# Optimization experiments

Hardware: AMD Instinct MI355X
Metric: run time of the kernel (lower is better)

## Reference

```python
import jax, jax.numpy as jnp
import numpy as np

D = 768          # n_embd
I = 3072         # moe_intermediate_size (4 * n_embd)
E = 8            # n_routed_experts
K = 2            # num_experts_per_tok
LIMIT = 10.0     # swiglu_limit
VOCAB = 32768


def setup_inputs() -> dict:
    key = jax.random.key(0)
    ks = jax.random.split(key, 10)
    s = 0.02
    return {
        "x": jax.random.normal(ks[0], (1, 2048, D), dtype=jnp.float32),
        "input_ids": jax.random.randint(ks[1], (1, 2048), 0, VOCAB, dtype=jnp.int64),
        "gate_w": jax.random.normal(ks[2], (D, E), dtype=jnp.float32) * s,
        "gate_bias": jnp.zeros((E,), dtype=jnp.float32),
        "w1": jax.random.normal(ks[3], (E, D, I), dtype=jnp.float32) * s,
        "w2": jax.random.normal(ks[4], (E, I, D), dtype=jnp.float32) * s,
        "w3": jax.random.normal(ks[5], (E, D, I), dtype=jnp.float32) * s,
        "w1s": jax.random.normal(ks[6], (D, I), dtype=jnp.float32) * s,
        "w2s": jax.random.normal(ks[7], (I, D), dtype=jnp.float32) * s,
        "w3s": jax.random.normal(ks[8], (D, I), dtype=jnp.float32) * s,
    }


def _expert(xf, W1, W2, W3):
    # SwiGLU with asymmetric clamping, as in DeepSeekExpert (swiglu_limit > 0)
    gate = jnp.minimum(xf @ W1, LIMIT)               # clamp max only
    up = jnp.clip(xf @ W3, -LIMIT, LIMIT)            # clamp both sides
    return (jax.nn.silu(gate) * up) @ W2


def reference(x, input_ids, gate_w, gate_bias, w1, w2, w3, w1s, w2s, w3s):
    B, T, _ = x.shape
    flat = x.reshape(-1, D)                           # [N, D], N = B*T
    N = flat.shape[0]

    # gating: sqrtsoftplus scoring
    scores = jnp.sqrt(jax.nn.softplus(flat @ gate_w))  # [N, E]
    routed_scores = scores + gate_bias                 # gate_bias used only for topk selection
    _, indices = jax.lax.top_k(routed_scores, K)       # [N, K]

    weights = jnp.take_along_axis(scores, indices, axis=1)  # [N, K]
    # norm_topk_prob=True; routed_scaling_factor=1.0
    weights = weights / jnp.clip(weights.sum(axis=-1, keepdims=True), 1e-6)

    # dense combine matrix [N, E] (jit-friendly dispatch/combine)
    combine = jnp.zeros((N, E), dtype=weights.dtype)
    combine = combine.at[jnp.arange(N)[:, None], indices].add(weights)

    # shared expert on all tokens
    y = _expert(flat, w1s, w2s, w3s)                   # [N, D]

    # routed experts: batched grouped GEMM over all tokens, then weighted combine
    gate_h = jnp.minimum(jnp.einsum('td,edi->eti', flat, w1), LIMIT)   # [E, N, I]
    up_h = jnp.clip(jnp.einsum('td,edi->eti', flat, w3), -LIMIT, LIMIT)
    h = jax.nn.silu(gate_h) * up_h                     # [E, N, I]
    out_e = jnp.einsum('eti,eid->etd', h, w2)          # [E, N, D]
    routed = jnp.einsum('etd,te->td', out_e, combine)  # [N, D]

    return (y + routed).reshape(B, T, D)
```

## Files before the change

kernel.cpp:

```cpp
#include <hip/hip_runtime.h>


#define D_ 768
#define I_ 3072
#define E_ 8
#define NTOK 2048
#define NPMAX 5120
#define MAXTILES 40
#define NSHT 16

typedef __bf16 bf16x8 __attribute__((ext_vector_type(8)));
typedef float floatx4 __attribute__((ext_vector_type(4)));

__device__ __forceinline__ unsigned short f2b(float f) {
    unsigned int u = __float_as_uint(f);
    u += 0x7fffu + ((u >> 16) & 1u);
    return (unsigned short)(u >> 16);
}


__global__ void tcast_kernel(const float* __restrict__ src,
                             unsigned short* __restrict__ dst, int R, int C) {
    __shared__ float t[32][33];
    const float* s = src + (size_t)blockIdx.z * R * C;
    unsigned short* d = dst + (size_t)blockIdx.z * R * C;
    int c0 = blockIdx.x * 32, r0 = blockIdx.y * 32;
    int tx = threadIdx.x & 31, ty = threadIdx.x >> 5;
#pragma unroll
    for (int j = 0; j < 4; j++) {
        int r = ty + j * 8;
        t[r][tx] = s[(size_t)(r0 + r) * C + c0 + tx];
    }
    __syncthreads();
#pragma unroll
    for (int j = 0; j < 4; j++) {
        int c = ty + j * 8;
        d[(size_t)(c0 + c) * R + r0 + tx] = f2b(t[tx][c]);
    }
}

__global__ void cast_x_kernel(const float* __restrict__ x,
                              unsigned short* __restrict__ xb) {
    int gid = blockIdx.x * 256 + threadIdx.x;
    float4 v = *(const float4*)(x + (size_t)gid * 4);
    ushort4 o;
    o.x = f2b(v.x); o.y = f2b(v.y); o.z = f2b(v.z); o.w = f2b(v.w);
    *(ushort4*)(xb + (size_t)gid * 4) = o;
}


__global__ void gate_topk_kernel(const float* __restrict__ x,
                                 const float* __restrict__ gw,
                                 const float* __restrict__ gb,
                                 int* __restrict__ idx, float* __restrict__ wts) {
    int t = blockIdx.x * 4 + (threadIdx.x >> 6);
    int lane = threadIdx.x & 63;
    float z[E_];
#pragma unroll
    for (int e = 0; e < E_; e++) z[e] = 0.f;
    const float* xr = x + (size_t)t * D_;
    for (int j = lane; j < D_; j += 64) {
        float xv = xr[j];
        const float* g = gw + (size_t)j * E_;
#pragma unroll
        for (int e = 0; e < E_; e++) z[e] += xv * g[e];
    }
#pragma unroll
    for (int off = 32; off > 0; off >>= 1)
#pragma unroll
        for (int e = 0; e < E_; e++) z[e] += __shfl_down(z[e], off, 64);
    if (lane == 0) {
        float s[E_], r[E_];
#pragma unroll
        for (int e = 0; e < E_; e++) {
            float zz = z[e];
            float sp = zz > 0.f ? zz + log1pf(expf(-zz)) : log1pf(expf(zz));
            s[e] = sqrtf(sp);
            r[e] = s[e] + gb[e];
        }
        int i0 = 0;
        for (int e = 1; e < E_; e++) if (r[e] > r[i0]) i0 = e;
        int i1 = (i0 == 0) ? 1 : 0;
        for (int e = 0; e < E_; e++) if (e != i0 && r[e] > r[i1]) i1 = e;
        float w0 = s[i0], w1 = s[i1];
        float inv = 1.f / fmaxf(w0 + w1, 1e-6f);
        idx[2 * t] = i0; idx[2 * t + 1] = i1;
        wts[2 * t] = w0 * inv; wts[2 * t + 1] = w1 * inv;
    }
}


__global__ void route_build_kernel(const int* __restrict__ idx,
                                   const float* __restrict__ wts,
                                   int* __restrict__ pair_token,
                                   float* __restrict__ pair_w,
                                   int* __restrict__ pos_of,
                                   int* __restrict__ tiles) {
    __shared__ int cnt[E_], seg[E_], cur[E_];
    int tid = threadIdx.x;
    if (tid < E_) { cnt[tid] = 0; cur[tid] = 0; }
    __syncthreads();
    for (int p = tid; p < NTOK * 2; p += 256) atomicAdd(&cnt[idx[p]], 1);
    __syncthreads();
    if (tid == 0) {
        int off = 0, nt = 0;
        for (int e = 0; e < E_; e++) {
            seg[e] = off;
            int te = (cnt[e] + 127) >> 7;
            for (int j = 0; j < te; j++) {
                tiles[nt * 2] = e; tiles[nt * 2 + 1] = off + j * 128; nt++;
            }
            off += te * 128;
        }
        for (; nt < MAXTILES; nt++) { tiles[nt * 2] = -1; tiles[nt * 2 + 1] = 0; }
    }
    for (int p = tid; p < NPMAX; p += 256) pair_token[p] = -1;
    __syncthreads();
    for (int p = tid; p < NTOK * 2; p += 256) {
        int e = idx[p];
        int r = atomicAdd(&cur[e], 1);
        int pos = seg[e] + r;
        pair_token[pos] = p >> 1;
        pair_w[pos] = wts[p];
        pos_of[p] = pos;
    }
}

__global__ void gather_kernel(const unsigned short* __restrict__ xb,
                              const int* __restrict__ pair_token,
                              unsigned short* __restrict__ xg) {
    int gid = blockIdx.x * 256 + threadIdx.x;
    int p = gid / (D_ / 8);
    int j = (gid % (D_ / 8)) * 8;
    int t = pair_token[p];
    int4 v = make_int4(0, 0, 0, 0);
    if (t >= 0) v = *(const int4*)(xb + (size_t)t * D_ + j);
    *(int4*)(xg + (size_t)p * D_ + j) = v;
}


__launch_bounds__(256)
__global__ void gemm_act_kernel(const unsigned short* __restrict__ xb,
                                const unsigned short* __restrict__ xg,
                                const unsigned short* __restrict__ w1sb,
                                const unsigned short* __restrict__ w3sb,
                                const unsigned short* __restrict__ w1b,
                                const unsigned short* __restrict__ w3b,
                                const int* __restrict__ tiles,
                                unsigned short* __restrict__ act_s,
                                unsigned short* __restrict__ act_r) {
    __shared__ __align__(16) unsigned short As[128 * 40];
    __shared__ __align__(16) unsigned short Bs1[64 * 40];
    __shared__ __align__(16) unsigned short Bs3[64 * 40];

    int mt = blockIdx.y;
    const unsigned short *A, *B1, *B3;
    unsigned short* C;
    int m0;
    if (mt < NSHT) {
        A = xb; B1 = w1sb; B3 = w3sb; C = act_s; m0 = mt * 128;
    } else {
        int e = tiles[(mt - NSHT) * 2];
        if (e < 0) return;
        m0 = tiles[(mt - NSHT) * 2 + 1];
        A = xg; B1 = w1b + (size_t)e * I_ * D_; B3 = w3b + (size_t)e * I_ * D_;
        C = act_r;
    }
    int n0 = blockIdx.x * 64;
    int tid = threadIdx.x;
    int lane = tid & 63, wave = tid >> 6;
    int wm = (wave & 1) * 64, wn = (wave >> 1) * 32;
    int l15 = lane & 15, quad = lane >> 4;

    int arow0 = tid >> 2, cc0 = (tid & 3) * 8;
    int arow1 = arow0 + 64;
    int brow = tid >> 2;

    floatx4 acc1[4][2] = {}; floatx4 acc3[4][2] = {};

    for (int k0 = 0; k0 < D_; k0 += 32) {
        __syncthreads();
        int4 va0 = *(const int4*)(A + (size_t)(m0 + arow0) * D_ + k0 + cc0);
        int4 va1 = *(const int4*)(A + (size_t)(m0 + arow1) * D_ + k0 + cc0);
        int4 vb1 = *(const int4*)(B1 + (size_t)(n0 + brow) * D_ + k0 + cc0);
        int4 vb3 = *(const int4*)(B3 + (size_t)(n0 + brow) * D_ + k0 + cc0);
        *(int4*)(As + arow0 * 40 + cc0) = va0;
        *(int4*)(As + arow1 * 40 + cc0) = va1;
        *(int4*)(Bs1 + brow * 40 + cc0) = vb1;
        *(int4*)(Bs3 + brow * 40 + cc0) = vb3;
        __syncthreads();

        bf16x8 af[4], b1f[2], b3f[2];
#pragma unroll
        for (int mi = 0; mi < 4; mi++)
            af[mi] = *(const bf16x8*)(As + (wm + mi * 16 + l15) * 40 + quad * 8);
#pragma unroll
        for (int ni = 0; ni < 2; ni++) {
            b1f[ni] = *(const bf16x8*)(Bs1 + (wn + ni * 16 + l15) * 40 + quad * 8);
            b3f[ni] = *(const bf16x8*)(Bs3 + (wn + ni * 16 + l15) * 40 + quad * 8);
        }
#pragma unroll
        for (int mi = 0; mi < 4; mi++)
#pragma unroll
            for (int ni = 0; ni < 2; ni++) {
                acc1[mi][ni] = __builtin_amdgcn_mfma_f32_16x16x32_bf16(
                    af[mi], b1f[ni], acc1[mi][ni], 0, 0, 0);
                acc3[mi][ni] = __builtin_amdgcn_mfma_f32_16x16x32_bf16(
                    af[mi], b3f[ni], acc3[mi][ni], 0, 0, 0);
            }
    }

#pragma unroll
    for (int mi = 0; mi < 4; mi++)
#pragma unroll
        for (int ni = 0; ni < 2; ni++) {
            int col = n0 + wn + ni * 16 + l15;
#pragma unroll
            for (int r = 0; r < 4; r++) {
                int row = m0 + wm + mi * 16 + quad * 4 + r;
                float g = fminf(acc1[mi][ni][r], 10.f);
                float u = fminf(fmaxf(acc3[mi][ni][r], -10.f), 10.f);
                float a = g / (1.f + __expf(-g)) * u;
                C[(size_t)row * I_ + col] = f2b(a);
            }
        }
}


__launch_bounds__(256)
__global__ void gemm_out_kernel(const unsigned short* __restrict__ act_s,
                                const unsigned short* __restrict__ act_r,
                                const unsigned short* __restrict__ w2sb,
                                const unsigned short* __restrict__ w2b,
                                const int* __restrict__ tiles,
                                float* __restrict__ y_s, float* __restrict__ ro) {
    __shared__ __align__(16) unsigned short As[128 * 40];
    __shared__ __align__(16) unsigned short Bs[64 * 40];

    int mt = blockIdx.y;
    const unsigned short *A, *B;
    float* C;
    int m0;
    if (mt < NSHT) {
        A = act_s; B = w2sb; C = y_s; m0 = mt * 128;
    } else {
        int e = tiles[(mt - NSHT) * 2];
        if (e < 0) return;
        m0 = tiles[(mt - NSHT) * 2 + 1];
        A = act_r; B = w2b + (size_t)e * I_ * D_; C = ro;
    }
    int n0 = blockIdx.x * 64;
    int tid = threadIdx.x;
    int lane = tid & 63, wave = tid >> 6;
    int wm = (wave & 1) * 64, wn = (wave >> 1) * 32;
    int l15 = lane & 15, quad = lane >> 4;

    int arow0 = tid >> 2, cc0 = (tid & 3) * 8;
    int arow1 = arow0 + 64;
    int brow = tid >> 2;

    floatx4 acc[4][2] = {};

    for (int k0 = 0; k0 < I_; k0 += 32) {
        __syncthreads();
        int4 va0 = *(const int4*)(A + (size_t)(m0 + arow0) * I_ + k0 + cc0);
        int4 va1 = *(const int4*)(A + (size_t)(m0 + arow1) * I_ + k0 + cc0);
        int4 vb  = *(const int4*)(B + (size_t)(n0 + brow) * I_ + k0 + cc0);
        *(int4*)(As + arow0 * 40 + cc0) = va0;
        *(int4*)(As + arow1 * 40 + cc0) = va1;
        *(int4*)(Bs + brow * 40 + cc0) = vb;
        __syncthreads();

        bf16x8 af[4], bf[2];
#pragma unroll
        for (int mi = 0; mi < 4; mi++)
            af[mi] = *(const bf16x8*)(As + (wm + mi * 16 + l15) * 40 + quad * 8);
#pragma unroll
        for (int ni = 0; ni < 2; ni++)
            bf[ni] = *(const bf16x8*)(Bs + (wn + ni * 16 + l15) * 40 + quad * 8);
#pragma unroll
        for (int mi = 0; mi < 4; mi++)
#pragma unroll
            for (int ni = 0; ni < 2; ni++)
                acc[mi][ni] = __builtin_amdgcn_mfma_f32_16x16x32_bf16(
                    af[mi], bf[ni], acc[mi][ni], 0, 0, 0);
    }

#pragma unroll
    for (int mi = 0; mi < 4; mi++)
#pragma unroll
        for (int ni = 0; ni < 2; ni++) {
            int col = n0 + wn + ni * 16 + l15;
#pragma unroll
            for (int r = 0; r < 4; r++) {
                int row = m0 + wm + mi * 16 + quad * 4 + r;
                C[(size_t)row * D_ + col] = acc[mi][ni][r];
            }
        }
}


__global__ void combine_kernel(const float* __restrict__ y_s,
                               const float* __restrict__ ro,
                               const int* __restrict__ pos_of,
                               const float* __restrict__ pair_w,
                               float* __restrict__ out) {
    int gid = blockIdx.x * 256 + threadIdx.x;
    int t = gid / (D_ / 4);
    int j = (gid % (D_ / 4)) * 4;
    int p0 = pos_of[2 * t], p1 = pos_of[2 * t + 1];
    float w0 = pair_w[p0], w1 = pair_w[p1];
    float4 a = *(const float4*)(y_s + (size_t)t * D_ + j);
    float4 b = *(const float4*)(ro + (size_t)p0 * D_ + j);
    float4 c = *(const float4*)(ro + (size_t)p1 * D_ + j);
    float4 o;
    o.x = a.x + w0 * b.x + w1 * c.x;
    o.y = a.y + w0 * b.y + w1 * c.y;
    o.z = a.z + w0 * b.z + w1 * c.z;
    o.w = a.w + w0 * b.w + w1 * c.w;
    *(float4*)(out + (size_t)t * D_ + j) = o;
}


extern "C" void kernel_launch(void* const* d_in, const int* in_sizes, int n_in,
                              void* d_out, int out_size, void* d_ws, size_t ws_size,
                              hipStream_t stream) {
    (void)in_sizes; (void)n_in; (void)out_size; (void)ws_size;
    const float* x   = (const float*)d_in[0];
    const float* gw  = (const float*)d_in[2];
    const float* gb  = (const float*)d_in[3];
    const float* w1  = (const float*)d_in[4];
    const float* w2  = (const float*)d_in[5];
    const float* w3  = (const float*)d_in[6];
    const float* w1s = (const float*)d_in[7];
    const float* w2s = (const float*)d_in[8];
    const float* w3s = (const float*)d_in[9];
    float* out = (float*)d_out;

    char* ws = (char*)d_ws;
    size_t off = 0;
    auto alloc = [&](size_t bytes) {
        size_t o = (off + 255) & ~(size_t)255;
        off = o + bytes;
        return (void*)(ws + o);
    };
    unsigned short* xb   = (unsigned short*)alloc((size_t)NTOK * D_ * 2);
    unsigned short* xg   = (unsigned short*)alloc((size_t)NPMAX * D_ * 2);
    unsigned short* w1b  = (unsigned short*)alloc((size_t)E_ * I_ * D_ * 2);
    unsigned short* w3b  = (unsigned short*)alloc((size_t)E_ * I_ * D_ * 2);
    unsigned short* w2b  = (unsigned short*)alloc((size_t)E_ * I_ * D_ * 2);
    unsigned short* w1sb = (unsigned short*)alloc((size_t)I_ * D_ * 2);
    unsigned short* w3sb = (unsigned short*)alloc((size_t)I_ * D_ * 2);
    unsigned short* w2sb = (unsigned short*)alloc((size_t)I_ * D_ * 2);
    unsigned short* acts = (unsigned short*)alloc((size_t)NTOK * I_ * 2);
    unsigned short* actr = (unsigned short*)alloc((size_t)NPMAX * I_ * 2);
    float* ys   = (float*)alloc((size_t)NTOK * D_ * 4);
    float* rout = (float*)alloc((size_t)NPMAX * D_ * 4);
    int*   idx  = (int*)alloc((size_t)NTOK * 2 * 4);
    float* wts  = (float*)alloc((size_t)NTOK * 2 * 4);
    int*   ptok = (int*)alloc((size_t)NPMAX * 4);
    float* pw   = (float*)alloc((size_t)NPMAX * 4);
    int*   posf = (int*)alloc((size_t)NTOK * 2 * 4);
    int*   tls  = (int*)alloc((size_t)MAXTILES * 2 * 4);

    tcast_kernel<<<dim3(I_ / 32, D_ / 32, E_), 256, 0, stream>>>(w1, w1b, D_, I_);
    tcast_kernel<<<dim3(I_ / 32, D_ / 32, E_), 256, 0, stream>>>(w3, w3b, D_, I_);
    tcast_kernel<<<dim3(D_ / 32, I_ / 32, E_), 256, 0, stream>>>(w2, w2b, I_, D_);
    tcast_kernel<<<dim3(I_ / 32, D_ / 32, 1), 256, 0, stream>>>(w1s, w1sb, D_, I_);
    tcast_kernel<<<dim3(I_ / 32, D_ / 32, 1), 256, 0, stream>>>(w3s, w3sb, D_, I_);
    tcast_kernel<<<dim3(D_ / 32, I_ / 32, 1), 256, 0, stream>>>(w2s, w2sb, I_, D_);

    cast_x_kernel<<<NTOK * D_ / 4 / 256, 256, 0, stream>>>(x, xb);
    gate_topk_kernel<<<NTOK / 4, 256, 0, stream>>>(x, gw, gb, idx, wts);
    route_build_kernel<<<1, 256, 0, stream>>>(idx, wts, ptok, pw, posf, tls);
    gather_kernel<<<NPMAX * (D_ / 8) / 256, 256, 0, stream>>>(xb, ptok, xg);

    gemm_act_kernel<<<dim3(I_ / 64, NSHT + MAXTILES), 256, 0, stream>>>(
        xb, xg, w1sb, w3sb, w1b, w3b, tls, acts, actr);
    gemm_out_kernel<<<dim3(D_ / 64, NSHT + MAXTILES), 256, 0, stream>>>(
        acts, actr, w2sb, w2b, tls, ys, rout);
    combine_kernel<<<NTOK * (D_ / 4) / 256, 256, 0, stream>>>(ys, rout, posf, pw, out);
}
```

Measured before the change: 519.4 us.

## Fuse prep kernels, gather in GEMM, 128x128 tiles with direct-to-LDS loads, split-K down-proj

Merges all weight transpose-casts, the x cast and gating into one prep kernel using 64x64 transpose tiles with vectorized stores. Removes the gather kernel by indexing token rows directly inside the gate/up GEMM. Both GEMMs move to 128x128 tiles loaded with global_load_lds into XOR-swizzled LDS. The down-projection is split four ways along K, writing bf16 partials that the combine kernel sums. The bf16 partial outputs lose some precision, and the partial buffers add extra memory traffic.

```diff
diff --git a/kernel.cpp b/kernel.cpp
--- a/kernel.cpp
+++ b/kernel.cpp
@@ -8,84 +8,112 @@
 #define NPMAX 5120
 #define MAXTILES 40
 #define NSHT 16
+#define SPLITK 4
+#define KS_ (I_ / SPLITK)
 
 typedef __bf16 bf16x8 __attribute__((ext_vector_type(8)));
 typedef float floatx4 __attribute__((ext_vector_type(4)));
+
+#define GLOAD_LDS16(g, l) __builtin_amdgcn_global_load_lds( \
+    (const __attribute__((address_space(1))) void*)(g),     \
+    (__attribute__((address_space(3))) void*)(l), 16, 0, 0)
 
 __device__ __forceinline__ unsigned short f2b(float f) {
     unsigned int u = __float_as_uint(f);
     u += 0x7fffu + ((u >> 16) & 1u);
     return (unsigned short)(u >> 16);
 }
-
-
-__global__ void tcast_kernel(const float* __restrict__ src,
-                             unsigned short* __restrict__ dst, int R, int C) {
-    __shared__ float t[32][33];
-    const float* s = src + (size_t)blockIdx.z * R * C;
-    unsigned short* d = dst + (size_t)blockIdx.z * R * C;
-    int c0 = blockIdx.x * 32, r0 = blockIdx.y * 32;
-    int tx = threadIdx.x & 31, ty = threadIdx.x >> 5;
-#pragma unroll
-    for (int j = 0; j < 4; j++) {
-        int r = ty + j * 8;
-        t[r][tx] = s[(size_t)(r0 + r) * C + c0 + tx];
-    }
-    __syncthreads();
-#pragma unroll
-    for (int j = 0; j < 4; j++) {
-        int c = ty + j * 8;
-        d[(size_t)(c0 + c) * R + r0 + tx] = f2b(t[tx][c]);
-    }
-}
-
-__global__ void cast_x_kernel(const float* __restrict__ x,
-                              unsigned short* __restrict__ xb) {
-    int gid = blockIdx.x * 256 + threadIdx.x;
-    float4 v = *(const float4*)(x + (size_t)gid * 4);
-    ushort4 o;
-    o.x = f2b(v.x); o.y = f2b(v.y); o.z = f2b(v.z); o.w = f2b(v.w);
-    *(ushort4*)(xb + (size_t)gid * 4) = o;
-}
-
-
-__global__ void gate_topk_kernel(const float* __restrict__ x,
-                                 const float* __restrict__ gw,
-                                 const float* __restrict__ gb,
-                                 int* __restrict__ idx, float* __restrict__ wts) {
-    int t = blockIdx.x * 4 + (threadIdx.x >> 6);
-    int lane = threadIdx.x & 63;
-    float z[E_];
-#pragma unroll
-    for (int e = 0; e < E_; e++) z[e] = 0.f;
-    const float* xr = x + (size_t)t * D_;
-    for (int j = lane; j < D_; j += 64) {
-        float xv = xr[j];
-        const float* g = gw + (size_t)j * E_;
-#pragma unroll
-        for (int e = 0; e < E_; e++) z[e] += xv * g[e];
-    }
-#pragma unroll
-    for (int off = 32; off > 0; off >>= 1)
-#pragma unroll
-        for (int e = 0; e < E_; e++) z[e] += __shfl_down(z[e], off, 64);
-    if (lane == 0) {
-        float s[E_], r[E_];
-#pragma unroll
-        for (int e = 0; e < E_; e++) {
-            float zz = z[e];
-            float sp = zz > 0.f ? zz + log1pf(expf(-zz)) : log1pf(expf(zz));
-            s[e] = sqrtf(sp);
-            r[e] = s[e] + gb[e];
-        }
-        int i0 = 0;
-        for (int e = 1; e < E_; e++) if (r[e] > r[i0]) i0 = e;
-        int i1 = (i0 == 0) ? 1 : 0;
-        for (int e = 0; e < E_; e++) if (e != i0 && r[e] > r[i1]) i1 = e;
-        float w0 = s[i0], w1 = s[i1];
-        float inv = 1.f / fmaxf(w0 + w1, 1e-6f);
-        idx[2 * t] = i0; idx[2 * t + 1] = i1;
-        wts[2 * t] = w0 * inv; wts[2 * t + 1] = w1 * inv;
+__device__ __forceinline__ float b2f(unsigned short u) {
+    return __uint_as_float((unsigned int)u << 16);
+}
+
+
+__global__ __launch_bounds__(256) void prep_kernel(
+    const float* __restrict__ x, const float* __restrict__ gw,
+    const float* __restrict__ gbias,
+    const float* __restrict__ w1, const float* __restrict__ w2,
+    const float* __restrict__ w3, const float* __restrict__ w1s,
+    const float* __restrict__ w2s, const float* __restrict__ w3s,
+    unsigned short* __restrict__ xb,
+    unsigned short* __restrict__ w1b, unsigned short* __restrict__ w3b,
+    unsigned short* __restrict__ w2b, unsigned short* __restrict__ w1sb,
+    unsigned short* __restrict__ w3sb, unsigned short* __restrict__ w2sb,
+    int* __restrict__ idx, float* __restrict__ wts) {
+    __shared__ float t[64][65];
+    int b = blockIdx.x, tid = threadIdx.x;
+    if (b < 15552) {
+        const float* s; unsigned short* d; int R, C, bx, by;
+        if (b < 10368) {
+            int z = b / 576, r = b % 576; bx = r % 48; by = r / 48; R = D_; C = I_;
+            if (z < 8)       { s = w1 + (size_t)z * D_ * I_;       d = w1b + (size_t)z * D_ * I_; }
+            else if (z < 16) { s = w3 + (size_t)(z - 8) * D_ * I_; d = w3b + (size_t)(z - 8) * D_ * I_; }
+            else if (z == 16){ s = w1s; d = w1sb; }
+            else             { s = w3s; d = w3sb; }
+        } else {
+            int bb = b - 10368;
+            int z = bb / 576, r = bb % 576; bx = r % 12; by = r / 12; R = I_; C = D_;
+            if (z < 8) { s = w2 + (size_t)z * I_ * D_; d = w2b + (size_t)z * I_ * D_; }
+            else       { s = w2s; d = w2sb; }
+        }
+        int c0 = bx * 64, r0 = by * 64;
+#pragma unroll
+        for (int j = 0; j < 4; j++) {
+            int slot = tid + j * 256;
+            int rr = slot >> 4, c4 = (slot & 15) * 4;
+            float4 v = *(const float4*)(s + (size_t)(r0 + rr) * C + c0 + c4);
+            t[rr][c4] = v.x; t[rr][c4 + 1] = v.y; t[rr][c4 + 2] = v.z; t[rr][c4 + 3] = v.w;
+        }
+        __syncthreads();
+#pragma unroll
+        for (int j = 0; j < 2; j++) {
+            int slot = tid + j * 256;
+            int c = slot >> 3, rs = (slot & 7) * 8;
+            unsigned short o[8] __attribute__((aligned(16)));
+#pragma unroll
+            for (int i = 0; i < 8; i++) o[i] = f2b(t[rs + i][c]);
+            *(int4*)(d + (size_t)(c0 + c) * R + r0 + rs) = *(const int4*)o;
+        }
+    } else if (b < 17088) {
+        int gid = (b - 15552) * 256 + tid;
+        float4 v = *(const float4*)(x + (size_t)gid * 4);
+        ushort4 o;
+        o.x = f2b(v.x); o.y = f2b(v.y); o.z = f2b(v.z); o.w = f2b(v.w);
+        *(ushort4*)(xb + (size_t)gid * 4) = o;
+    } else {
+        int tok = (b - 17088) * 4 + (tid >> 6);
+        int lane = tid & 63;
+        float z[E_];
+#pragma unroll
+        for (int e = 0; e < E_; e++) z[e] = 0.f;
+        const float* xr = x + (size_t)tok * D_;
+        for (int j = lane; j < D_; j += 64) {
+            float xv = xr[j];
+            const float* g = gw + (size_t)j * E_;
+#pragma unroll
+            for (int e = 0; e < E_; e++) z[e] += xv * g[e];
+        }
+#pragma unroll
+        for (int off = 32; off > 0; off >>= 1)
+#pragma unroll
+            for (int e = 0; e < E_; e++) z[e] += __shfl_down(z[e], off, 64);
+        if (lane == 0) {
+            float s[E_], r[E_];
+#pragma unroll
+            for (int e = 0; e < E_; e++) {
+                float zz = z[e];
+                float sp = zz > 0.f ? zz + log1pf(expf(-zz)) : log1pf(expf(zz));
+                s[e] = sqrtf(sp);
+                r[e] = s[e] + gbias[e];
+            }
+            int i0 = 0;
+            for (int e = 1; e < E_; e++) if (r[e] > r[i0]) i0 = e;
+            int i1 = (i0 == 0) ? 1 : 0;
+            for (int e = 0; e < E_; e++) if (e != i0 && r[e] > r[i1]) i1 = e;
+            float w0 = s[i0], w1v = s[i1];
+            float inv = 1.f / fmaxf(w0 + w1v, 1e-6f);
+            idx[2 * tok] = i0; idx[2 * tok + 1] = i1;
+            wts[2 * tok] = w0 * inv; wts[2 * tok + 1] = w1v * inv;
+        }
     }
 }
 
@@ -126,83 +154,86 @@
     }
 }
 
-__global__ void gather_kernel(const unsigned short* __restrict__ xb,
-                              const int* __restrict__ pair_token,
-                              unsigned short* __restrict__ xg) {
-    int gid = blockIdx.x * 256 + threadIdx.x;
-    int p = gid / (D_ / 8);
-    int j = (gid % (D_ / 8)) * 8;
-    int t = pair_token[p];
-    int4 v = make_int4(0, 0, 0, 0);
-    if (t >= 0) v = *(const int4*)(xb + (size_t)t * D_ + j);
-    *(int4*)(xg + (size_t)p * D_ + j) = v;
-}
-
 
 __launch_bounds__(256)
 __global__ void gemm_act_kernel(const unsigned short* __restrict__ xb,
-                                const unsigned short* __restrict__ xg,
                                 const unsigned short* __restrict__ w1sb,
                                 const unsigned short* __restrict__ w3sb,
                                 const unsigned short* __restrict__ w1b,
                                 const unsigned short* __restrict__ w3b,
                                 const int* __restrict__ tiles,
+                                const int* __restrict__ pair_token,
                                 unsigned short* __restrict__ act_s,
                                 unsigned short* __restrict__ act_r) {
-    __shared__ __align__(16) unsigned short As[128 * 40];
-    __shared__ __align__(16) unsigned short Bs1[64 * 40];
-    __shared__ __align__(16) unsigned short Bs3[64 * 40];
+    __shared__ __align__(16) unsigned short As[128 * 32];
+    __shared__ __align__(16) unsigned short Bs1[128 * 32];
+    __shared__ __align__(16) unsigned short Bs3[128 * 32];
 
     int mt = blockIdx.y;
-    const unsigned short *A, *B1, *B3;
+    const unsigned short *B1, *B3;
     unsigned short* C;
-    int m0;
+    int m0; bool routed;
     if (mt < NSHT) {
-        A = xb; B1 = w1sb; B3 = w3sb; C = act_s; m0 = mt * 128;
+        B1 = w1sb; B3 = w3sb; C = act_s; m0 = mt * 128; routed = false;
     } else {
         int e = tiles[(mt - NSHT) * 2];
         if (e < 0) return;
         m0 = tiles[(mt - NSHT) * 2 + 1];
-        A = xg; B1 = w1b + (size_t)e * I_ * D_; B3 = w3b + (size_t)e * I_ * D_;
-        C = act_r;
-    }
-    int n0 = blockIdx.x * 64;
+        B1 = w1b + (size_t)e * I_ * D_; B3 = w3b + (size_t)e * I_ * D_;
+        C = act_r; routed = true;
+    }
+    int n0 = blockIdx.x * 128;
     int tid = threadIdx.x;
     int lane = tid & 63, wave = tid >> 6;
-    int wm = (wave & 1) * 64, wn = (wave >> 1) * 32;
+    int wm = (wave & 1) * 64, wn = (wave >> 1) * 64;
     int l15 = lane & 15, quad = lane >> 4;
 
-    int arow0 = tid >> 2, cc0 = (tid & 3) * 8;
-    int arow1 = arow0 + 64;
-    int brow = tid >> 2;
-
-    floatx4 acc1[4][2] = {}; floatx4 acc3[4][2] = {};
+    int r = tid >> 2;
+    int lc8 = (((tid & 3) ^ ((r >> 1) & 3)) * 8);
+    int tokA0, tokA1;
+    if (routed) {
+        tokA0 = pair_token[m0 + r];      if (tokA0 < 0) tokA0 = 0;
+        tokA1 = pair_token[m0 + r + 64]; if (tokA1 < 0) tokA1 = 0;
+    } else { tokA0 = m0 + r; tokA1 = m0 + r + 64; }
+    const unsigned short* ApA0 = xb + (size_t)tokA0 * D_ + lc8;
+    const unsigned short* ApA1 = xb + (size_t)tokA1 * D_ + lc8;
+    const unsigned short* B1p0 = B1 + (size_t)(n0 + r) * D_ + lc8;
+    const unsigned short* B1p1 = B1 + (size_t)(n0 + r + 64) * D_ + lc8;
+    const unsigned short* B3p0 = B3 + (size_t)(n0 + r) * D_ + lc8;
+    const unsigned short* B3p1 = B3 + (size_t)(n0 + r + 64) * D_ + lc8;
+    unsigned short* lA0  = As  + wave * 512;
+    unsigned short* lA1  = As  + 2048 + wave * 512;
+    unsigned short* lB10 = Bs1 + wave * 512;
+    unsigned short* lB11 = Bs1 + 2048 + wave * 512;
+    unsigned short* lB30 = Bs3 + wave * 512;
+    unsigned short* lB31 = Bs3 + 2048 + wave * 512;
+
+    int swz = (quad ^ ((l15 >> 1) & 3)) * 8;
+    floatx4 acc1[4][4] = {}; floatx4 acc3[4][4] = {};
 
     for (int k0 = 0; k0 < D_; k0 += 32) {
         __syncthreads();
-        int4 va0 = *(const int4*)(A + (size_t)(m0 + arow0) * D_ + k0 + cc0);
-        int4 va1 = *(const int4*)(A + (size_t)(m0 + arow1) * D_ + k0 + cc0);
-        int4 vb1 = *(const int4*)(B1 + (size_t)(n0 + brow) * D_ + k0 + cc0);
-        int4 vb3 = *(const int4*)(B3 + (size_t)(n0 + brow) * D_ + k0 + cc0);
-        *(int4*)(As + arow0 * 40 + cc0) = va0;
-        *(int4*)(As + arow1 * 40 + cc0) = va1;
-        *(int4*)(Bs1 + brow * 40 + cc0) = vb1;
-        *(int4*)(Bs3 + brow * 40 + cc0) = vb3;
+        GLOAD_LDS16(ApA0 + k0, lA0);
+        GLOAD_LDS16(ApA1 + k0, lA1);
+        GLOAD_LDS16(B1p0 + k0, lB10);
+        GLOAD_LDS16(B1p1 + k0, lB11);
+        GLOAD_LDS16(B3p0 + k0, lB30);
+        GLOAD_LDS16(B3p1 + k0, lB31);
         __syncthreads();
 
-        bf16x8 af[4], b1f[2], b3f[2];
+        bf16x8 af[4], b1f[4], b3f[4];
 #pragma unroll
         for (int mi = 0; mi < 4; mi++)
-            af[mi] = *(const bf16x8*)(As + (wm + mi * 16 + l15) * 40 + quad * 8);
-#pragma unroll
-        for (int ni = 0; ni < 2; ni++) {
-            b1f[ni] = *(const bf16x8*)(Bs1 + (wn + ni * 16 + l15) * 40 + quad * 8);
-            b3f[ni] = *(const bf16x8*)(Bs3 + (wn + ni * 16 + l15) * 40 + quad * 8);
+            af[mi] = *(const bf16x8*)(As + (wm + mi * 16 + l15) * 32 + swz);
+#pragma unroll
+        for (int ni = 0; ni < 4; ni++) {
+            b1f[ni] = *(const bf16x8*)(Bs1 + (wn + ni * 16 + l15) * 32 + swz);
+            b3f[ni] = *(const bf16x8*)(Bs3 + (wn + ni * 16 + l15) * 32 + swz);
         }
 #pragma unroll
         for (int mi = 0; mi < 4; mi++)
 #pragma unroll
-            for (int ni = 0; ni < 2; ni++) {
+            for (int ni = 0; ni < 4; ni++) {
                 acc1[mi][ni] = __builtin_amdgcn_mfma_f32_16x16x32_bf16(
                     af[mi], b1f[ni], acc1[mi][ni], 0, 0, 0);
                 acc3[mi][ni] = __builtin_amdgcn_mfma_f32_16x16x32_bf16(
@@ -213,13 +244,13 @@
 #pragma unroll
     for (int mi = 0; mi < 4; mi++)
 #pragma unroll
-        for (int ni = 0; ni < 2; ni++) {
+        for (int ni = 0; ni < 4; ni++) {
             int col = n0 + wn + ni * 16 + l15;
 #pragma unroll
-            for (int r = 0; r < 4; r++) {
-                int row = m0 + wm + mi * 16 + quad * 4 + r;
-                float g = fminf(acc1[mi][ni][r], 10.f);
-                float u = fminf(fmaxf(acc3[mi][ni][r], -10.f), 10.f);
+            for (int rr = 0; rr < 4; rr++) {
+                int row = m0 + wm + mi * 16 + quad * 4 + rr;
+                float g = fminf(acc1[mi][ni][rr], 10.f);
+                float u = fminf(fmaxf(acc3[mi][ni][rr], -10.f), 10.f);
                 float a = g / (1.f + __expf(-g)) * u;
                 C[(size_t)row * I_ + col] = f2b(a);
             }
@@ -233,55 +264,63 @@
                                 const unsigned short* __restrict__ w2sb,
                                 const unsigned short* __restrict__ w2b,
                                 const int* __restrict__ tiles,
-                                float* __restrict__ y_s, float* __restrict__ ro) {
-    __shared__ __align__(16) unsigned short As[128 * 40];
-    __shared__ __align__(16) unsigned short Bs[64 * 40];
-
-    int mt = blockIdx.y;
+                                unsigned short* __restrict__ ysp,
+                                unsigned short* __restrict__ rop) {
+    __shared__ __align__(16) unsigned short As[128 * 32];
+    __shared__ __align__(16) unsigned short Bs[128 * 32];
+
+    int mt = blockIdx.y, ks = blockIdx.z;
+    int kbase = ks * KS_;
     const unsigned short *A, *B;
-    float* C;
+    unsigned short* C;
     int m0;
     if (mt < NSHT) {
-        A = act_s; B = w2sb; C = y_s; m0 = mt * 128;
+        A = act_s; B = w2sb; C = ysp + (size_t)ks * NTOK * D_; m0 = mt * 128;
     } else {
         int e = tiles[(mt - NSHT) * 2];
         if (e < 0) return;
         m0 = tiles[(mt - NSHT) * 2 + 1];
-        A = act_r; B = w2b + (size_t)e * I_ * D_; C = ro;
-    }
-    int n0 = blockIdx.x * 64;
+        A = act_r; B = w2b + (size_t)e * I_ * D_; C = rop + (size_t)ks * NPMAX * D_;
+    }
+    int n0 = blockIdx.x * 128;
     int tid = threadIdx.x;
     int lane = tid & 63, wave = tid >> 6;
-    int wm = (wave & 1) * 64, wn = (wave >> 1) * 32;
+    int wm = (wave & 1) * 64, wn = (wave >> 1) * 64;
     int l15 = lane & 15, quad = lane >> 4;
 
-    int arow0 = tid >> 2, cc0 = (tid & 3) * 8;
-    int arow1 = arow0 + 64;
-    int brow = tid >> 2;
-
-    floatx4 acc[4][2] = {};
-
-    for (int k0 = 0; k0 < I_; k0 += 32) {
+    int r = tid >> 2;
+    int lc8 = (((tid & 3) ^ ((r >> 1) & 3)) * 8);
+    const unsigned short* Ap0 = A + (size_t)(m0 + r) * I_ + kbase + lc8;
+    const unsigned short* Ap1 = A + (size_t)(m0 + r + 64) * I_ + kbase + lc8;
+    const unsigned short* Bp0 = B + (size_t)(n0 + r) * I_ + kbase + lc8;
+    const unsigned short* Bp1 = B + (size_t)(n0 + r + 64) * I_ + kbase + lc8;
+    unsigned short* lA0 = As + wave * 512;
+    unsigned short* lA1 = As + 2048 + wave * 512;
+    unsigned short* lB0 = Bs + wave * 512;
+    unsigned short* lB1 = Bs + 2048 + wave * 512;
+
+    int swz = (quad ^ ((l15 >> 1) & 3)) * 8;
+    floatx4 acc[4][4] = {};
+
+    for (int k0 = 0; k0 < KS_; k0 += 32) {
         __syncthreads();
-        int4 va0 = *(const int4*)(A + (size_t)(m0 + arow0) * I_ + k0 + cc0);
-        int4 va1 = *(const int4*)(A + (size_t)(m0 + arow1) * I_ + k0 + cc0);
-        int4 vb  = *(const int4*)(B + (size_t)(n0 + brow) * I_ + k0 + cc0);
-        *(int4*)(As + arow0 * 40 + cc0) = va0;
-        *(int4*)(As + arow1 * 40 + cc0) = va1;
-        *(int4*)(Bs + brow * 40 + cc0) = vb;
+        GLOAD_LDS16(Ap0 + k0, lA0);
+        GLOAD_LDS16(Ap1 + k0, lA1);
+        GLOAD_LDS16(Bp0 + k0, lB0);
+        GLOAD_LDS16(Bp1 + k0, lB1);
         __syncthreads();
 
-        bf16x8 af[4], bf[2];
+        bf16x8 af[4], bf[4];
 #pragma unroll
         for (int mi = 0; mi < 4; mi++)
-            af[mi] = *(const bf16x8*)(As + (wm + mi * 16 + l15) * 40 + quad * 8);
-#pragma unroll
-        for (int ni = 0; ni < 2; ni++)
-            bf[ni] = *(const bf16x8*)(Bs + (wn + ni * 16 + l15) * 40 + quad * 8);
+            af[mi] = *(const bf16x8*)(As + (wm + mi * 16 + l15) * 32 + swz);
+#pragma unroll
+        for (int ni = 0; ni < 4; ni++)
+            bf[ni] = *(const bf16x8*)(Bs + (wn + ni * 16 + l15) * 32 + swz);
 #pragma unroll
         for (int mi = 0; mi < 4; mi++)
 #pragma unroll
-            for (int ni = 0; ni < 2; ni++)
+            for (int ni = 0; ni < 4; ni++)
                 acc[mi][ni] = __builtin_amdgcn_mfma_f32_16x16x32_bf16(
                     af[mi], bf[ni], acc[mi][ni], 0, 0, 0);
     }
@@ -289,19 +328,19 @@
 #pragma unroll
     for (int mi = 0; mi < 4; mi++)
 #pragma unroll
-        for (int ni = 0; ni < 2; ni++) {
+        for (int ni = 0; ni < 4; ni++) {
             int col = n0 + wn + ni * 16 + l15;
 #pragma unroll
-            for (int r = 0; r < 4; r++) {
-                int row = m0 + wm + mi * 16 + quad * 4 + r;
-                C[(size_t)row * D_ + col] = acc[mi][ni][r];
+            for (int rr = 0; rr < 4; rr++) {
+                int row = m0 + wm + mi * 16 + quad * 4 + rr;
+                C[(size_t)row * D_ + col] = f2b(acc[mi][ni][rr]);
             }
         }
 }
 
 
-__global__ void combine_kernel(const float* __restrict__ y_s,
-                               const float* __restrict__ ro,
+__global__ void combine_kernel(const unsigned short* __restrict__ ysp,
+                               const unsigned short* __restrict__ rop,
                                const int* __restrict__ pos_of,
                                const float* __restrict__ pair_w,
                                float* __restrict__ out) {
@@ -310,14 +349,18 @@
     int j = (gid % (D_ / 4)) * 4;
     int p0 = pos_of[2 * t], p1 = pos_of[2 * t + 1];
     float w0 = pair_w[p0], w1 = pair_w[p1];
-    float4 a = *(const float4*)(y_s + (size_t)t * D_ + j);
-    float4 b = *(const float4*)(ro + (size_t)p0 * D_ + j);
-    float4 c = *(const float4*)(ro + (size_t)p1 * D_ + j);
-    float4 o;
-    o.x = a.x + w0 * b.x + w1 * c.x;
-    o.y = a.y + w0 * b.y + w1 * c.y;
-    o.z = a.z + w0 * b.z + w1 * c.z;
-    o.w = a.w + w0 * b.w + w1 * c.w;
+    float a0 = 0.f, a1 = 0.f, a2 = 0.f, a3 = 0.f;
+#pragma unroll
+    for (int ks = 0; ks < SPLITK; ks++) {
+        ushort4 a = *(const ushort4*)(ysp + ((size_t)ks * NTOK + t) * D_ + j);
+        ushort4 b = *(const ushort4*)(rop + ((size_t)ks * NPMAX + p0) * D_ + j);
+        ushort4 c = *(const ushort4*)(rop + ((size_t)ks * NPMAX + p1) * D_ + j);
+        a0 += b2f(a.x) + w0 * b2f(b.x) + w1 * b2f(c.x);
+        a1 += b2f(a.y) + w0 * b2f(b.y) + w1 * b2f(c.y);
+        a2 += b2f(a.z) + w0 * b2f(b.z) + w1 * b2f(c.z);
+        a3 += b2f(a.w) + w0 * b2f(b.w) + w1 * b2f(c.w);
+    }
+    float4 o; o.x = a0; o.y = a1; o.z = a2; o.w = a3;
     *(float4*)(out + (size_t)t * D_ + j) = o;
 }
 
@@ -345,7 +388,6 @@
         return (void*)(ws + o);
     };
     unsigned short* xb   = (unsigned short*)alloc((size_t)NTOK * D_ * 2);
-    unsigned short* xg   = (unsigned short*)alloc((size_t)NPMAX * D_ * 2);
     unsigned short* w1b  = (unsigned short*)alloc((size_t)E_ * I_ * D_ * 2);
     unsigned short* w3b  = (unsigned short*)alloc((size_t)E_ * I_ * D_ * 2);
     unsigned short* w2b  = (unsigned short*)alloc((size_t)E_ * I_ * D_ * 2);
@@ -354,8 +396,8 @@
     unsigned short* w2sb = (unsigned short*)alloc((size_t)I_ * D_ * 2);
     unsigned short* acts = (unsigned short*)alloc((size_t)NTOK * I_ * 2);
     unsigned short* actr = (unsigned short*)alloc((size_t)NPMAX * I_ * 2);
-    float* ys   = (float*)alloc((size_t)NTOK * D_ * 4);
-    float* rout = (float*)alloc((size_t)NPMAX * D_ * 4);
+    unsigned short* ysp  = (unsigned short*)alloc((size_t)SPLITK * NTOK * D_ * 2);
+    unsigned short* rop  = (unsigned short*)alloc((size_t)SPLITK * NPMAX * D_ * 2);
     int*   idx  = (int*)alloc((size_t)NTOK * 2 * 4);
     float* wts  = (float*)alloc((size_t)NTOK * 2 * 4);
     int*   ptok = (int*)alloc((size_t)NPMAX * 4);
@@ -363,21 +405,13 @@
     int*   posf = (int*)alloc((size_t)NTOK * 2 * 4);
     int*   tls  = (int*)alloc((size_t)MAXTILES * 2 * 4);
 
-    tcast_kernel<<<dim3(I_ / 32, D_ / 32, E_), 256, 0, stream>>>(w1, w1b, D_, I_);
-    tcast_kernel<<<dim3(I_ / 32, D_ / 32, E_), 256, 0, stream>>>(w3, w3b, D_, I_);
-    tcast_kernel<<<dim3(D_ / 32, I_ / 32, E_), 256, 0, stream>>>(w2, w2b, I_, D_);
-    tcast_kernel<<<dim3(I_ / 32, D_ / 32, 1), 256, 0, stream>>>(w1s, w1sb, D_, I_);
-    tcast_kernel<<<dim3(I_ / 32, D_ / 32, 1), 256, 0, stream>>>(w3s, w3sb, D_, I_);
-    tcast_kernel<<<dim3(D_ / 32, I_ / 32, 1), 256, 0, stream>>>(w2s, w2sb, I_, D_);
-
-    cast_x_kernel<<<NTOK * D_ / 4 / 256, 256, 0, stream>>>(x, xb);
-    gate_topk_kernel<<<NTOK / 4, 256, 0, stream>>>(x, gw, gb, idx, wts);
+    prep_kernel<<<17600, 256, 0, stream>>>(x, gw, gb, w1, w2, w3, w1s, w2s, w3s,
+                                           xb, w1b, w3b, w2b, w1sb, w3sb, w2sb,
+                                           idx, wts);
     route_build_kernel<<<1, 256, 0, stream>>>(idx, wts, ptok, pw, posf, tls);
-    gather_kernel<<<NPMAX * (D_ / 8) / 256, 256, 0, stream>>>(xb, ptok, xg);
-
-    gemm_act_kernel<<<dim3(I_ / 64, NSHT + MAXTILES), 256, 0, stream>>>(
-        xb, xg, w1sb, w3sb, w1b, w3b, tls, acts, actr);
-    gemm_out_kernel<<<dim3(D_ / 64, NSHT + MAXTILES), 256, 0, stream>>>(
-        acts, actr, w2sb, w2b, tls, ys, rout);
-    combine_kernel<<<NTOK * (D_ / 4) / 256, 256, 0, stream>>>(ys, rout, posf, pw, out);
-}
+    gemm_act_kernel<<<dim3(I_ / 128, NSHT + MAXTILES), 256, 0, stream>>>(
+        xb, w1sb, w3sb, w1b, w3b, tls, ptok, acts, actr);
+    gemm_out_kernel<<<dim3(D_ / 128, NSHT + MAXTILES, SPLITK), 256, 0, stream>>>(
+        acts, actr, w2sb, w2b, tls, ysp, rop);
+    combine_kernel<<<NTOK * (D_ / 4) / 256, 256, 0, stream>>>(ysp, rop, posf, pw, out);
+}
```

After: 522.7 us. No clear change (+0.6%).
